# Kernel tuning notes

Measured on AMD Instinct MI355X. Metric: run time of the kernel, lower is better.

The kernel has to match this reference:

```python
import jax, jax.numpy as jnp
import numpy as np
from jax import lax

D_MODEL = 768
D_STATE = 64
BATCH = 2
SEQ = 2048


def setup_inputs() -> dict:
    key = jax.random.key(0)
    ks = jax.random.split(key, 12)
    d, n = D_MODEL, D_STATE
    x = jax.random.normal(ks[0], (BATCH, SEQ, d), dtype=jnp.float32)
    ln_gamma = jnp.ones((d,), jnp.float32)
    ln_beta = jnp.zeros((d,), jnp.float32)
    # nn.Linear default init ~ U(-1/sqrt(d), 1/sqrt(d))
    s = 1.0 / np.sqrt(d)
    W_in = jax.random.uniform(ks[1], (d, d), jnp.float32, -s, s)
    b_in = jax.random.uniform(ks[2], (d,), jnp.float32, -s, s)
    log_A = jax.random.normal(ks[3], (d, n), jnp.float32)
    B_p = jax.random.normal(ks[4], (d, n), jnp.float32) * 0.1
    C_p = jax.random.normal(ks[5], (d, n), jnp.float32) * 0.1
    D_p = jnp.ones((d,), jnp.float32)
    log_dt = jax.random.uniform(ks[6], (d,), jnp.float32) * 0.01 - 2.0
    W_out = jax.random.uniform(ks[7], (d, d), jnp.float32, -s, s)
    b_out = jax.random.uniform(ks[8], (d,), jnp.float32, -s, s)
    return {
        "x": x, "ln_gamma": ln_gamma, "ln_beta": ln_beta,
        "W_in": W_in, "b_in": b_in, "log_A": log_A,
        "B_p": B_p, "C_p": C_p, "D_p": D_p, "log_dt": log_dt,
        "W_out": W_out, "b_out": b_out,
    }


def reference(x, ln_gamma, ln_beta, W_in, b_in, log_A, B_p, C_p, D_p, log_dt, W_out, b_out):
    residual = x
    # LayerNorm (eps=1e-5, elementwise affine)
    mu = jnp.mean(x, axis=-1, keepdims=True)
    var = jnp.var(x, axis=-1, keepdims=True)
    xn = (x - mu) / jnp.sqrt(var + 1e-5) * ln_gamma + ln_beta
    # in_proj (torch Linear: x @ W^T + b)
    u = xn @ W_in.T + b_in  # [B,S,d]
    # Discretization
    A = -jnp.exp(log_A)                     # [d,N]
    dt = jnp.exp(log_dt)[:, None]           # [d,1]
    A_bar = jnp.exp(dt * A)                 # [d,N]
    B_bar = B_p * dt                        # [d,N]
    b, s, d = u.shape
    h0 = jnp.zeros((b, d, D_STATE), u.dtype)
    u_t = jnp.transpose(u, (1, 0, 2))       # [S,B,d]

    def step(h, xt):
        # h: [B,d,N], xt: [B,d]
        h = A_bar * h + B_bar * xt[:, :, None]
        y = jnp.einsum('bdn,dn->bd', h, C_p) + D_p * xt
        return h, y

    _, ys = lax.scan(step, h0, u_t)         # ys: [S,B,d]
    y = jnp.transpose(ys, (1, 0, 2))        # [B,S,d]
    y = y @ W_out.T + b_out
    # dropout is identity in eval mode
    return y + residual
```

## Files before the change

kernel.cpp:

```cpp
#include <hip/hip_runtime.h>
#include <math.h>

#define D_MODEL 768
#define D_STATE 64
#define BATCH   2
#define SEQ     2048
#define M_TOTAL (BATCH * SEQ)

typedef unsigned short ushort_t;
typedef float f32x4 __attribute__((ext_vector_type(4)));
typedef __bf16 bf16x8 __attribute__((ext_vector_type(8)));

__device__ __forceinline__ ushort_t f2bf(float f) {
    unsigned u = __float_as_uint(f);
    u = (u + 0x7FFFu + ((u >> 16) & 1u)) >> 16;
    return (ushort_t)u;
}

__device__ __forceinline__ void gload16(const void* g, void* shm) {
    __builtin_amdgcn_global_load_lds(
        (const __attribute__((address_space(1))) void*)g,
        (__attribute__((address_space(3))) void*)shm, 16, 0, 0);
}

__global__ __launch_bounds__(256) void pre_kernel(const float* __restrict__ x,
                                                  const float* __restrict__ gamma,
                                                  const float* __restrict__ beta,
                                                  ushort_t* __restrict__ xnb,
                                                  const float* __restrict__ W_in,
                                                  const float* __restrict__ W_out,
                                                  ushort_t* __restrict__ Winb,
                                                  ushort_t* __restrict__ Woutb) {
    int bx = blockIdx.x;
    if (bx >= 1024) {
        int b2 = bx - 1024;
        const float* src = (b2 < 576) ? W_in : W_out;
        ushort_t*    dst = (b2 < 576) ? Winb : Woutb;
        int blk = (b2 < 576) ? b2 : b2 - 576;
        int i = (blk * 256 + threadIdx.x) * 4;
        float4 v = *(const float4*)(src + i);
        ushort4 o = make_ushort4(f2bf(v.x), f2bf(v.y), f2bf(v.z), f2bf(v.w));
        *(ushort4*)(dst + i) = o;
        return;
    }
    int row  = bx * 4 + (threadIdx.x >> 6);
    int lane = threadIdx.x & 63;
    const float* xr = x + (size_t)row * D_MODEL;
    float4 v[3];
    v[0] = *(const float4*)(xr + lane * 4);
    v[1] = *(const float4*)(xr + 256 + lane * 4);
    v[2] = *(const float4*)(xr + 512 + lane * 4);
    float s = 0.f, ss = 0.f;
#pragma unroll
    for (int i = 0; i < 3; ++i) {
        s  += v[i].x + v[i].y + v[i].z + v[i].w;
        ss += v[i].x * v[i].x + v[i].y * v[i].y + v[i].z * v[i].z + v[i].w * v[i].w;
    }
#pragma unroll
    for (int off = 1; off < 64; off <<= 1) {
        s  += __shfl_xor(s, off, 64);
        ss += __shfl_xor(ss, off, 64);
    }
    float mean = s * (1.0f / 768.0f);
    float var  = ss * (1.0f / 768.0f) - mean * mean;
    float inv  = 1.0f / sqrtf(var + 1e-5f);
    ushort_t* xo = xnb + (size_t)row * D_MODEL;
#pragma unroll
    for (int i = 0; i < 3; ++i) {
        int c = i * 256 + lane * 4;
        float4 g  = *(const float4*)(gamma + c);
        float4 bb = *(const float4*)(beta + c);
        ushort4 o = make_ushort4(f2bf((v[i].x - mean) * inv * g.x + bb.x),
                                 f2bf((v[i].y - mean) * inv * g.y + bb.y),
                                 f2bf((v[i].z - mean) * inv * g.z + bb.z),
                                 f2bf((v[i].w - mean) * inv * g.w + bb.w));
        *(ushort4*)(xo + c) = o;
    }
}


__global__ __launch_bounds__(256) void gemm_in(const ushort_t* __restrict__ A,
                                               const ushort_t* __restrict__ B,
                                               const float* __restrict__ bias,
                                               ushort_t* __restrict__ uTb) {
    __shared__ __align__(16) char smem[32768];
    float* T = (float*)smem;

    int tid = threadIdx.x;
    int w = tid >> 6, l = tid & 63;
    int bm = blockIdx.x * 64, bn = blockIdx.y * 64;
    int mq = (w & 1) * 32, nq = (w >> 1) * 32;

    int rowq = l >> 4;
    int segq = l & 15;

    float biasv[2];
#pragma unroll
    for (int nt = 0; nt < 2; ++nt)
        biasv[nt] = bias[bn + nq + nt * 16 + (l & 15)];

    f32x4 acc[2][2] = {};
    for (int k0 = 0; k0 < D_MODEL; k0 += 128) {
#pragma unroll
        for (int q = 0; q < 4; ++q) {
            int row = w * 16 + q * 4 + rowq;
            int col = k0 + ((segq ^ (row & 7)) * 8);
            gload16(A + (size_t)(bm + row) * D_MODEL + col, smem + w * 4096 + q * 1024);
            gload16(B + (size_t)(bn + row) * D_MODEL + col, smem + 16384 + w * 4096 + q * 1024);
        }
        __syncthreads();
#pragma unroll
        for (int kk = 0; kk < 4; ++kk) {
            int sgb = kk * 4 + (l >> 4);
            bf16x8 af[2], bf[2];
#pragma unroll
            for (int mt = 0; mt < 2; ++mt) {
                int r = mq + mt * 16 + (l & 15);
                af[mt] = *(const bf16x8*)(smem + r * 256 + ((sgb ^ (r & 7)) * 16));
            }
#pragma unroll
            for (int nt = 0; nt < 2; ++nt) {
                int r = nq + nt * 16 + (l & 15);
                bf[nt] = *(const bf16x8*)(smem + 16384 + r * 256 + ((sgb ^ (r & 7)) * 16));
            }
#pragma unroll
            for (int mt = 0; mt < 2; ++mt)
#pragma unroll
                for (int nt = 0; nt < 2; ++nt)
                    acc[mt][nt] = __builtin_amdgcn_mfma_f32_16x16x32_bf16(af[mt], bf[nt], acc[mt][nt], 0, 0, 0);
        }
        __syncthreads();
    }
#pragma unroll
    for (int mt = 0; mt < 2; ++mt)
#pragma unroll
        for (int nt = 0; nt < 2; ++nt)
#pragma unroll
            for (int i = 0; i < 4; ++i) {
                int nl = nq + nt * 16 + (l & 15);
                int ml = mq + mt * 16 + (l >> 4) * 4 + i;
                T[nl * 68 + ml] = acc[mt][nt][i] + biasv[nt];
            }
    __syncthreads();
    int b = bm >> 11, sbase = bm & 2047;
    int n = tid >> 2, mseg = (tid & 3) * 16;
    ushort_t* dst = uTb + ((size_t)b * D_MODEL + bn + n) * SEQ + sbase + mseg;
#pragma unroll
    for (int q = 0; q < 4; ++q) {
        float4 v = *(const float4*)&T[n * 68 + mseg + q * 4];
        ushort4 o = make_ushort4(f2bf(v.x), f2bf(v.y), f2bf(v.z), f2bf(v.w));
        *(ushort4*)(dst + q * 4) = o;
    }
}

__global__ __launch_bounds__(256) void gemm_out(const ushort_t* __restrict__ A,
                                                const ushort_t* __restrict__ B,
                                                const float* __restrict__ bias,
                                                const float* __restrict__ resid,
                                                float* __restrict__ out) {
    __shared__ __align__(16) char smem[32768];
    int tid = threadIdx.x;
    int w = tid >> 6, l = tid & 63;
    int bm = blockIdx.x * 64, bn = blockIdx.y * 64;
    int mq = (w & 1) * 32, nq = (w >> 1) * 32;

    int rowq = l >> 4;
    int segq = l & 15;

    float biasv[2];
#pragma unroll
    for (int nt = 0; nt < 2; ++nt)
        biasv[nt] = bias[bn + nq + nt * 16 + (l & 15)];

    f32x4 acc[2][2] = {};
    for (int k0 = 0; k0 < D_MODEL; k0 += 128) {
#pragma unroll
        for (int q = 0; q < 4; ++q) {
            int row = w * 16 + q * 4 + rowq;
            int col = k0 + ((segq ^ (row & 7)) * 8);
            gload16(A + (size_t)(bm + row) * D_MODEL + col, smem + w * 4096 + q * 1024);
            gload16(B + (size_t)(bn + row) * D_MODEL + col, smem + 16384 + w * 4096 + q * 1024);
        }
        __syncthreads();
#pragma unroll
        for (int kk = 0; kk < 4; ++kk) {
            int sgb = kk * 4 + (l >> 4);
            bf16x8 af[2], bf[2];
#pragma unroll
            for (int mt = 0; mt < 2; ++mt) {
                int r = mq + mt * 16 + (l & 15);
                af[mt] = *(const bf16x8*)(smem + r * 256 + ((sgb ^ (r & 7)) * 16));
            }
#pragma unroll
            for (int nt = 0; nt < 2; ++nt) {
                int r = nq + nt * 16 + (l & 15);
                bf[nt] = *(const bf16x8*)(smem + 16384 + r * 256 + ((sgb ^ (r & 7)) * 16));
            }
#pragma unroll
            for (int mt = 0; mt < 2; ++mt)
#pragma unroll
                for (int nt = 0; nt < 2; ++nt)
                    acc[mt][nt] = __builtin_amdgcn_mfma_f32_16x16x32_bf16(af[mt], bf[nt], acc[mt][nt], 0, 0, 0);
        }
        __syncthreads();
    }
#pragma unroll
    for (int mt = 0; mt < 2; ++mt)
#pragma unroll
        for (int i = 0; i < 4; ++i) {
            int m = bm + mq + mt * 16 + (l >> 4) * 4 + i;
            const float* rp = resid + (size_t)m * D_MODEL + bn;
            float* op = out + (size_t)m * D_MODEL + bn;
#pragma unroll
            for (int nt = 0; nt < 2; ++nt) {
                int nl = nq + nt * 16 + (l & 15);
                op[nl] = acc[mt][nt][i] + biasv[nt] + rp[nl];
            }
        }
}

#define OFF_U  0
#define OFF_V  9216
#define OFF_T  18432
#define OFF_M  27648
#define OFF_H  36864
#define OFF_W  46080
#define OFF_SM 63488

__global__ __launch_bounds__(256) void scan_mm(const ushort_t* __restrict__ uTb,
                                               const float* __restrict__ log_A,
                                               const float* __restrict__ B_p,
                                               const float* __restrict__ C_p,
                                               const float* __restrict__ D_p,
                                               const float* __restrict__ log_dt,
                                               float* __restrict__ yT) {
    __shared__ __align__(16) char smem[65024];
    ushort_t* Up = (ushort_t*)(smem + OFF_U);
    ushort_t* Vp = (ushort_t*)(smem + OFF_V);
    ushort_t* Tp = (ushort_t*)(smem + OFF_T);
    ushort_t* Mp = (ushort_t*)(smem + OFF_M);
    ushort_t* Hp = (ushort_t*)(smem + OFF_H);
    float*    Wp = (float*)(smem + OFF_W);
    float*    Kp = (float*)(smem + OFF_W);
    float*    aArr  = (float*)(smem + OFF_SM);
    float*    BbArr = aArr + 64;
    float*    CcArr = aArr + 128;
    float*    CBArr = aArr + 192;
    float*    Kc    = aArr + 256;

    int d   = blockIdx.x;
    int tid = threadIdx.x;
    int w   = tid >> 6, l = tid & 63;

    if (tid < 64) {
        int n = tid;
        float dt = __expf(log_dt[d]);
        float a  = -dt * __expf(log_A[d * 64 + n]);
        float Bb = B_p[d * 64 + n] * dt;
        float Cc = C_p[d * 64 + n];
        aArr[n] = a; BbArr[n] = Bb; CcArr[n] = Cc; CBArr[n] = Cc * Bb;
    }
    __syncthreads();

    {
        int tau = tid & 63, part = tid >> 6;
        float s = 0.f;
#pragma unroll
        for (int i = 0; i < 16; ++i) {
            int n = part * 16 + i;
            s += CBArr[n] * __expf((float)tau * aArr[n]);
        }
        Kp[part * 64 + tau] = s;
    }
    __syncthreads();
    if (tid < 64)
        Kc[tid] = Kp[tid] + Kp[64 + tid] + Kp[128 + tid] + Kp[192 + tid]
                + (tid == 0 ? D_p[d] : 0.f);
    __syncthreads();

    {
        int r = tid >> 2, seg = (tid & 3) * 16;
        float a = aArr[r], Bb = BbArr[r];
#pragma unroll
        for (int i = 0; i < 16; ++i) {
            int s = seg + i;
            Vp[r * 72 + s] = f2bf(Bb * __expf((float)(63 - s) * a));
        }
#pragma unroll
        for (int i = 0; i < 16; ++i) {
            int n = seg + i;
            Mp[r * 72 + n] = f2bf(CcArr[n] * __expf((float)(r + 1) * aArr[n]));
        }
#pragma unroll
        for (int i = 0; i < 16; ++i) {
            int s = seg + i;
            Tp[r * 72 + s] = (s <= r) ? f2bf(Kc[r - s]) : (ushort_t)0;
        }
        int col = r, bu = col >> 5, cu = col & 31;
        const ushort_t* usrc = uTb + ((size_t)bu * D_MODEL + d) * SEQ + cu * 64 + seg;
        *(uint4*)(Up + col * 72 + seg)     = *(const uint4*)(usrc);
        *(uint4*)(Up + col * 72 + seg + 8) = *(const uint4*)(usrc + 8);
    }
    __syncthreads();

    {
        int p0 = w * 16;
        f32x4 acc1[4] = {};
#pragma unroll
        for (int kk = 0; kk < 2; ++kk) {
            int koff = kk * 32 + (l >> 4) * 8;
            bf16x8 af = *(const bf16x8*)(Vp + (p0 + (l & 15)) * 72 + koff);
#pragma unroll
            for (int qt = 0; qt < 4; ++qt) {
                bf16x8 bf = *(const bf16x8*)(Up + (qt * 16 + (l & 15)) * 72 + koff);
                acc1[qt] = __builtin_amdgcn_mfma_f32_16x16x32_bf16(af, bf, acc1[qt], 0, 0, 0);
            }
        }
#pragma unroll
        for (int qt = 0; qt < 4; ++qt)
#pragma unroll
            for (int i = 0; i < 4; ++i)
                Wp[(qt * 16 + (l & 15)) * 68 + p0 + (l >> 4) * 4 + i] = acc1[qt][i];
    }
    __syncthreads();

    if (tid < 128) {
        int b2 = tid >> 6, n = tid & 63;
        float Ab64 = __expf(64.f * aArr[n]);
        float H = 0.f;
#pragma unroll
        for (int c = 0; c < 32; ++c) {
            int col = b2 * 32 + c;
            Hp[col * 72 + n] = f2bf(H);
            H = fmaf(Ab64, H, Wp[col * 68 + n]);
        }
    }
    __syncthreads();

    {
        int j0 = w * 16;
        f32x4 accY[4] = {};
#pragma unroll
        for (int kk = 0; kk < 2; ++kk) {
            int koff = kk * 32 + (l >> 4) * 8;
            bf16x8 at = *(const bf16x8*)(Tp + (j0 + (l & 15)) * 72 + koff);
            bf16x8 am = *(const bf16x8*)(Mp + (j0 + (l & 15)) * 72 + koff);
#pragma unroll
            for (int qt = 0; qt < 4; ++qt) {
                bf16x8 bu = *(const bf16x8*)(Up + (qt * 16 + (l & 15)) * 72 + koff);
                bf16x8 bh = *(const bf16x8*)(Hp + (qt * 16 + (l & 15)) * 72 + koff);
                accY[qt] = __builtin_amdgcn_mfma_f32_16x16x32_bf16(at, bu, accY[qt], 0, 0, 0);
                accY[qt] = __builtin_amdgcn_mfma_f32_16x16x32_bf16(am, bh, accY[qt], 0, 0, 0);
            }
        }
#pragma unroll
        for (int qt = 0; qt < 4; ++qt)
#pragma unroll
            for (int i = 0; i < 4; ++i)
                Wp[(qt * 16 + (l & 15)) * 68 + j0 + (l >> 4) * 4 + i] = accY[qt][i];
    }
    __syncthreads();

    {
        int col = tid >> 2, jseg = (tid & 3) * 16;
        int b3 = col >> 5, c3 = col & 31;
        float* dst = yT + ((size_t)b3 * D_MODEL + d) * SEQ + c3 * 64 + jseg;
#pragma unroll
        for (int q = 0; q < 4; ++q)
            *(float4*)(dst + q * 4) = *(const float4*)(Wp + col * 68 + jseg + q * 4);
    }
}

__global__ __launch_bounds__(256) void tcast_kernel(const float* __restrict__ yT,
                                                    ushort_t* __restrict__ yA) {
    __shared__ float T2[64 * 68];
    int t = threadIdx.x;
    int s0 = blockIdx.x * 64, d0 = blockIdx.y * 64, b = blockIdx.z;
    int dl = t >> 2, sq = (t & 3) * 16;
    const float* src = yT + ((size_t)b * D_MODEL + d0 + dl) * SEQ + s0 + sq;
#pragma unroll
    for (int q = 0; q < 4; ++q) {
        float4 v = *(const float4*)(src + q * 4);
        T2[(sq + q * 4 + 0) * 68 + dl] = v.x;
        T2[(sq + q * 4 + 1) * 68 + dl] = v.y;
        T2[(sq + q * 4 + 2) * 68 + dl] = v.z;
        T2[(sq + q * 4 + 3) * 68 + dl] = v.w;
    }
    __syncthreads();
    int sl = t >> 2, dseg = (t & 3) * 16;
    ushort_t* dst = yA + ((size_t)(b * SEQ + s0 + sl)) * D_MODEL + d0 + dseg;
#pragma unroll
    for (int q = 0; q < 4; ++q) {
        float4 v = *(const float4*)&T2[sl * 68 + dseg + q * 4];
        ushort4 o = make_ushort4(f2bf(v.x), f2bf(v.y), f2bf(v.z), f2bf(v.w));
        *(ushort4*)(dst + q * 4) = o;
    }
}

extern "C" void kernel_launch(void* const* d_in, const int* in_sizes, int n_in,
                              void* d_out, int out_size, void* d_ws, size_t ws_size,
                              hipStream_t stream) {
    const float* x        = (const float*)d_in[0];
    const float* ln_gamma = (const float*)d_in[1];
    const float* ln_beta  = (const float*)d_in[2];
    const float* W_in     = (const float*)d_in[3];
    const float* b_in     = (const float*)d_in[4];
    const float* log_A    = (const float*)d_in[5];
    const float* B_p      = (const float*)d_in[6];
    const float* C_p      = (const float*)d_in[7];
    const float* D_p      = (const float*)d_in[8];
    const float* log_dt   = (const float*)d_in[9];
    const float* W_out    = (const float*)d_in[10];
    const float* b_out    = (const float*)d_in[11];
    float* out = (float*)d_out;

    char* ws = (char*)d_ws;
    ushort_t* uTb   = (ushort_t*)(ws + 0);
    float*    yT    = (float*)(ws + 6291456);
    ushort_t* xnb   = (ushort_t*)(ws + 18874368);
    ushort_t* yA    = xnb;
    ushort_t* Winb  = (ushort_t*)(ws + 25165824);
    ushort_t* Woutb = (ushort_t*)(ws + 26345472);

    pre_kernel<<<dim3(1024 + 1152), 256, 0, stream>>>(x, ln_gamma, ln_beta, xnb,
                                                      W_in, W_out, Winb, Woutb);
    gemm_in<<<dim3(M_TOTAL / 64, D_MODEL / 64), 256, 0, stream>>>(xnb, Winb, b_in, uTb);
    scan_mm<<<dim3(D_MODEL), 256, 0, stream>>>(uTb, log_A, B_p, C_p, D_p, log_dt, yT);
    tcast_kernel<<<dim3(SEQ / 64, D_MODEL / 64, BATCH), 256, 0, stream>>>(yT, yA);
    gemm_out<<<dim3(M_TOTAL / 64, D_MODEL / 64), 256, 0, stream>>>(yA, Woutb, b_out, x, out);
}
```

Baseline: 129.2 us.

## Use double-buffered 128x96 GEMM tiles and store scan output as bf16

Both projection GEMMs now share a core that uses larger 128x96 block tiles with 64x48 per-wave tiles and double-buffers the K=64 slices in LDS, so the next slice is prefetched while the current one is multiplied. This raises per-block data reuse and hides global load latency, at the cost of more registers, fewer blocks (256 vs 768) and a launch bound of one block per CU. The scan kernel now writes its transposed output as bf16 instead of fp32, halving that intermediate's traffic and simplifying the transpose kernel to a pure bf16 shuffle. The gemm_in epilogue also converts to bf16 in LDS before wider 16-byte stores.

```diff
diff --git a/kernel.cpp b/kernel.cpp
--- a/kernel.cpp
+++ b/kernel.cpp
@@ -78,143 +78,124 @@
     }
 }
 
-
-__global__ __launch_bounds__(256) void gemm_in(const ushort_t* __restrict__ A,
-                                               const ushort_t* __restrict__ B,
-                                               const float* __restrict__ bias,
-                                               ushort_t* __restrict__ uTb) {
-    __shared__ __align__(16) char smem[32768];
-    float* T = (float*)smem;
-
+#define ABUF  16384
+#define BUFSZ 28672
+
+__device__ __forceinline__ void gemm_core(const ushort_t* __restrict__ A,
+                                          const ushort_t* __restrict__ B,
+                                          const float* __restrict__ bias,
+                                          char* smem, int tid, int bm, int bn,
+                                          int w, int l, int wm, int wn,
+                                          f32x4 acc[4][3], float biasv[3]) {
+    int seg8 = ((l & 7) ^ (l >> 3)) * 8;
+    const ushort_t* gA = A + (size_t)(bm + w * 32 + (l >> 3)) * D_MODEL + seg8;
+    const ushort_t* gB = B + (size_t)(bn + w * 24 + (l >> 3)) * D_MODEL + seg8;
+#pragma unroll
+    for (int nt = 0; nt < 3; ++nt)
+        biasv[nt] = bias[bn + wn + nt * 16 + (l & 15)];
+#pragma unroll
+    for (int q = 0; q < 4; ++q)
+        gload16(gA + (size_t)(q * 8) * D_MODEL, smem + (w * 32 + q * 8) * 128);
+#pragma unroll
+    for (int q = 0; q < 3; ++q)
+        gload16(gB + (size_t)(q * 8) * D_MODEL, smem + ABUF + (w * 24 + q * 8) * 128);
+    __syncthreads();
+    for (int it = 0; it < 12; ++it) {
+        const char* cb = smem + (it & 1) * BUFSZ;
+        if (it < 11) {
+            char* nb = smem + ((it + 1) & 1) * BUFSZ;
+            int k = (it + 1) * 64;
+#pragma unroll
+            for (int q = 0; q < 4; ++q)
+                gload16(gA + (size_t)(q * 8) * D_MODEL + k, nb + (w * 32 + q * 8) * 128);
+#pragma unroll
+            for (int q = 0; q < 3; ++q)
+                gload16(gB + (size_t)(q * 8) * D_MODEL + k, nb + ABUF + (w * 24 + q * 8) * 128);
+        }
+#pragma unroll
+        for (int kk = 0; kk < 2; ++kk) {
+            int sgb = kk * 4 + (l >> 4);
+            bf16x8 af[4], bf[3];
+#pragma unroll
+            for (int mt = 0; mt < 4; ++mt) {
+                int r = wm + mt * 16 + (l & 15);
+                af[mt] = *(const bf16x8*)(cb + r * 128 + ((sgb ^ (r & 7)) * 16));
+            }
+#pragma unroll
+            for (int nt = 0; nt < 3; ++nt) {
+                int r = wn + nt * 16 + (l & 15);
+                bf[nt] = *(const bf16x8*)(cb + ABUF + r * 128 + ((sgb ^ (r & 7)) * 16));
+            }
+#pragma unroll
+            for (int mt = 0; mt < 4; ++mt)
+#pragma unroll
+                for (int nt = 0; nt < 3; ++nt)
+                    acc[mt][nt] = __builtin_amdgcn_mfma_f32_16x16x32_bf16(af[mt], bf[nt], acc[mt][nt], 0, 0, 0);
+        }
+        __syncthreads();
+    }
+}
+
+__global__ __launch_bounds__(256, 1) void gemm_in(const ushort_t* __restrict__ A,
+                                                  const ushort_t* __restrict__ B,
+                                                  const float* __restrict__ bias,
+                                                  ushort_t* __restrict__ uTb) {
+    __shared__ __align__(16) char smem[2 * BUFSZ];
     int tid = threadIdx.x;
     int w = tid >> 6, l = tid & 63;
-    int bm = blockIdx.x * 64, bn = blockIdx.y * 64;
-    int mq = (w & 1) * 32, nq = (w >> 1) * 32;
-
-    int rowq = l >> 4;
-    int segq = l & 15;
-
-    float biasv[2];
-#pragma unroll
-    for (int nt = 0; nt < 2; ++nt)
-        biasv[nt] = bias[bn + nq + nt * 16 + (l & 15)];
-
-    f32x4 acc[2][2] = {};
-    for (int k0 = 0; k0 < D_MODEL; k0 += 128) {
-#pragma unroll
-        for (int q = 0; q < 4; ++q) {
-            int row = w * 16 + q * 4 + rowq;
-            int col = k0 + ((segq ^ (row & 7)) * 8);
-            gload16(A + (size_t)(bm + row) * D_MODEL + col, smem + w * 4096 + q * 1024);
-            gload16(B + (size_t)(bn + row) * D_MODEL + col, smem + 16384 + w * 4096 + q * 1024);
-        }
-        __syncthreads();
-#pragma unroll
-        for (int kk = 0; kk < 4; ++kk) {
-            int sgb = kk * 4 + (l >> 4);
-            bf16x8 af[2], bf[2];
-#pragma unroll
-            for (int mt = 0; mt < 2; ++mt) {
-                int r = mq + mt * 16 + (l & 15);
-                af[mt] = *(const bf16x8*)(smem + r * 256 + ((sgb ^ (r & 7)) * 16));
-            }
-#pragma unroll
-            for (int nt = 0; nt < 2; ++nt) {
-                int r = nq + nt * 16 + (l & 15);
-                bf[nt] = *(const bf16x8*)(smem + 16384 + r * 256 + ((sgb ^ (r & 7)) * 16));
-            }
-#pragma unroll
-            for (int mt = 0; mt < 2; ++mt)
-#pragma unroll
-                for (int nt = 0; nt < 2; ++nt)
-                    acc[mt][nt] = __builtin_amdgcn_mfma_f32_16x16x32_bf16(af[mt], bf[nt], acc[mt][nt], 0, 0, 0);
-        }
-        __syncthreads();
-    }
-#pragma unroll
-    for (int mt = 0; mt < 2; ++mt)
-#pragma unroll
-        for (int nt = 0; nt < 2; ++nt)
+    int bm = blockIdx.x * 128, bn = blockIdx.y * 96;
+    int wm = (w & 1) * 64, wn = (w >> 1) * 48;
+    f32x4 acc[4][3] = {};
+    float biasv[3];
+    gemm_core(A, B, bias, smem, tid, bm, bn, w, l, wm, wn, acc, biasv);
+
+    ushort_t* T = (ushort_t*)smem;
+#pragma unroll
+    for (int mt = 0; mt < 4; ++mt)
+#pragma unroll
+        for (int nt = 0; nt < 3; ++nt)
 #pragma unroll
             for (int i = 0; i < 4; ++i) {
-                int nl = nq + nt * 16 + (l & 15);
-                int ml = mq + mt * 16 + (l >> 4) * 4 + i;
-                T[nl * 68 + ml] = acc[mt][nt][i] + biasv[nt];
-            }
-    __syncthreads();
-    int b = bm >> 11, sbase = bm & 2047;
-    int n = tid >> 2, mseg = (tid & 3) * 16;
-    ushort_t* dst = uTb + ((size_t)b * D_MODEL + bn + n) * SEQ + sbase + mseg;
-#pragma unroll
-    for (int q = 0; q < 4; ++q) {
-        float4 v = *(const float4*)&T[n * 68 + mseg + q * 4];
-        ushort4 o = make_ushort4(f2bf(v.x), f2bf(v.y), f2bf(v.z), f2bf(v.w));
-        *(ushort4*)(dst + q * 4) = o;
-    }
-}
-
-__global__ __launch_bounds__(256) void gemm_out(const ushort_t* __restrict__ A,
-                                                const ushort_t* __restrict__ B,
-                                                const float* __restrict__ bias,
-                                                const float* __restrict__ resid,
-                                                float* __restrict__ out) {
-    __shared__ __align__(16) char smem[32768];
+                int n = wn + nt * 16 + (l & 15);
+                int m = wm + mt * 16 + (l >> 4) * 4 + i;
+                T[n * 136 + m] = f2bf(acc[mt][nt][i] + biasv[nt]);
+            }
+    __syncthreads();
+    int b = bm >> 11, s0 = bm & 2047;
+#pragma unroll
+    for (int rep = 0; rep < 6; ++rep) {
+        int idx = rep * 256 + tid;
+        int row = idx >> 4, sg = idx & 15;
+        uint4 v = *(const uint4*)&T[row * 136 + sg * 8];
+        *(uint4*)(uTb + ((size_t)b * D_MODEL + bn + row) * SEQ + s0 + sg * 8) = v;
+    }
+}
+
+__global__ __launch_bounds__(256, 1) void gemm_out(const ushort_t* __restrict__ A,
+                                                   const ushort_t* __restrict__ B,
+                                                   const float* __restrict__ bias,
+                                                   const float* __restrict__ resid,
+                                                   float* __restrict__ out) {
+    __shared__ __align__(16) char smem[2 * BUFSZ];
     int tid = threadIdx.x;
     int w = tid >> 6, l = tid & 63;
-    int bm = blockIdx.x * 64, bn = blockIdx.y * 64;
-    int mq = (w & 1) * 32, nq = (w >> 1) * 32;
-
-    int rowq = l >> 4;
-    int segq = l & 15;
-
-    float biasv[2];
-#pragma unroll
-    for (int nt = 0; nt < 2; ++nt)
-        biasv[nt] = bias[bn + nq + nt * 16 + (l & 15)];
-
-    f32x4 acc[2][2] = {};
-    for (int k0 = 0; k0 < D_MODEL; k0 += 128) {
-#pragma unroll
-        for (int q = 0; q < 4; ++q) {
-            int row = w * 16 + q * 4 + rowq;
-            int col = k0 + ((segq ^ (row & 7)) * 8);
-            gload16(A + (size_t)(bm + row) * D_MODEL + col, smem + w * 4096 + q * 1024);
-            gload16(B + (size_t)(bn + row) * D_MODEL + col, smem + 16384 + w * 4096 + q * 1024);
-        }
-        __syncthreads();
-#pragma unroll
-        for (int kk = 0; kk < 4; ++kk) {
-            int sgb = kk * 4 + (l >> 4);
-            bf16x8 af[2], bf[2];
-#pragma unroll
-            for (int mt = 0; mt < 2; ++mt) {
-                int r = mq + mt * 16 + (l & 15);
-                af[mt] = *(const bf16x8*)(smem + r * 256 + ((sgb ^ (r & 7)) * 16));
-            }
-#pragma unroll
-            for (int nt = 0; nt < 2; ++nt) {
-                int r = nq + nt * 16 + (l & 15);
-                bf[nt] = *(const bf16x8*)(smem + 16384 + r * 256 + ((sgb ^ (r & 7)) * 16));
-            }
-#pragma unroll
-            for (int mt = 0; mt < 2; ++mt)
-#pragma unroll
-                for (int nt = 0; nt < 2; ++nt)
-                    acc[mt][nt] = __builtin_amdgcn_mfma_f32_16x16x32_bf16(af[mt], bf[nt], acc[mt][nt], 0, 0, 0);
-        }
-        __syncthreads();
-    }
-#pragma unroll
-    for (int mt = 0; mt < 2; ++mt)
+    int bm = blockIdx.x * 128, bn = blockIdx.y * 96;
+    int wm = (w & 1) * 64, wn = (w >> 1) * 48;
+    f32x4 acc[4][3] = {};
+    float biasv[3];
+    gemm_core(A, B, bias, smem, tid, bm, bn, w, l, wm, wn, acc, biasv);
+
+#pragma unroll
+    for (int mt = 0; mt < 4; ++mt)
 #pragma unroll
         for (int i = 0; i < 4; ++i) {
-            int m = bm + mq + mt * 16 + (l >> 4) * 4 + i;
+            int m = bm + wm + mt * 16 + (l >> 4) * 4 + i;
             const float* rp = resid + (size_t)m * D_MODEL + bn;
             float* op = out + (size_t)m * D_MODEL + bn;
 #pragma unroll
-            for (int nt = 0; nt < 2; ++nt) {
-                int nl = nq + nt * 16 + (l & 15);
-                op[nl] = acc[mt][nt][i] + biasv[nt] + rp[nl];
+            for (int nt = 0; nt < 3; ++nt) {
+                int n = wn + nt * 16 + (l & 15);
+                op[n] = acc[mt][nt][i] + biasv[nt] + rp[n];
             }
         }
 }
@@ -233,7 +214,7 @@
                                                const float* __restrict__ C_p,
                                                const float* __restrict__ D_p,
                                                const float* __restrict__ log_dt,
-                                               float* __restrict__ yT) {
+                                               ushort_t* __restrict__ yTb) {
     __shared__ __align__(16) char smem[65024];
     ushort_t* Up = (ushort_t*)(smem + OFF_U);
     ushort_t* Vp = (ushort_t*)(smem + OFF_V);
@@ -364,37 +345,34 @@
     {
         int col = tid >> 2, jseg = (tid & 3) * 16;
         int b3 = col >> 5, c3 = col & 31;
-        float* dst = yT + ((size_t)b3 * D_MODEL + d) * SEQ + c3 * 64 + jseg;
-#pragma unroll
-        for (int q = 0; q < 4; ++q)
-            *(float4*)(dst + q * 4) = *(const float4*)(Wp + col * 68 + jseg + q * 4);
-    }
-}
-
-__global__ __launch_bounds__(256) void tcast_kernel(const float* __restrict__ yT,
+        ushort_t* dst = yTb + ((size_t)b3 * D_MODEL + d) * SEQ + c3 * 64 + jseg;
+#pragma unroll
+        for (int q = 0; q < 4; ++q) {
+            float4 v = *(const float4*)(Wp + col * 68 + jseg + q * 4);
+            ushort4 o = make_ushort4(f2bf(v.x), f2bf(v.y), f2bf(v.z), f2bf(v.w));
+            *(ushort4*)(dst + q * 4) = o;
+        }
+    }
+}
+
+__global__ __launch_bounds__(256) void tcast_kernel(const ushort_t* __restrict__ yTb,
                                                     ushort_t* __restrict__ yA) {
-    __shared__ float T2[64 * 68];
+    __shared__ ushort_t T3[64 * 72];
     int t = threadIdx.x;
     int s0 = blockIdx.x * 64, d0 = blockIdx.y * 64, b = blockIdx.z;
     int dl = t >> 2, sq = (t & 3) * 16;
-    const float* src = yT + ((size_t)b * D_MODEL + d0 + dl) * SEQ + s0 + sq;
-#pragma unroll
-    for (int q = 0; q < 4; ++q) {
-        float4 v = *(const float4*)(src + q * 4);
-        T2[(sq + q * 4 + 0) * 68 + dl] = v.x;
-        T2[(sq + q * 4 + 1) * 68 + dl] = v.y;
-        T2[(sq + q * 4 + 2) * 68 + dl] = v.z;
-        T2[(sq + q * 4 + 3) * 68 + dl] = v.w;
-    }
+    const ushort_t* src = yTb + ((size_t)b * D_MODEL + d0 + dl) * SEQ + s0 + sq;
+    ushort_t tmp[16];
+    *(uint4*)tmp       = *(const uint4*)src;
+    *(uint4*)(tmp + 8) = *(const uint4*)(src + 8);
+#pragma unroll
+    for (int i = 0; i < 16; ++i)
+        T3[(sq + i) * 72 + dl] = tmp[i];
     __syncthreads();
     int sl = t >> 2, dseg = (t & 3) * 16;
-    ushort_t* dst = yA + ((size_t)(b * SEQ + s0 + sl)) * D_MODEL + d0 + dseg;
-#pragma unroll
-    for (int q = 0; q < 4; ++q) {
-        float4 v = *(const float4*)&T2[sl * 68 + dseg + q * 4];
-        ushort4 o = make_ushort4(f2bf(v.x), f2bf(v.y), f2bf(v.z), f2bf(v.w));
-        *(ushort4*)(dst + q * 4) = o;
-    }
+    ushort_t* dst = yA + ((size_t)b * SEQ + s0 + sl) * D_MODEL + d0 + dseg;
+    *(uint4*)dst       = *(const uint4*)&T3[sl * 72 + dseg];
+    *(uint4*)(dst + 8) = *(const uint4*)&T3[sl * 72 + dseg + 8];
 }
 
 extern "C" void kernel_launch(void* const* d_in, const int* in_sizes, int n_in,
@@ -416,16 +394,16 @@
 
     char* ws = (char*)d_ws;
     ushort_t* uTb   = (ushort_t*)(ws + 0);
-    float*    yT    = (float*)(ws + 6291456);
-    ushort_t* xnb   = (ushort_t*)(ws + 18874368);
+    ushort_t* yTb   = (ushort_t*)(ws + 6291456);
+    ushort_t* xnb   = (ushort_t*)(ws + 12582912);
     ushort_t* yA    = xnb;
-    ushort_t* Winb  = (ushort_t*)(ws + 25165824);
-    ushort_t* Woutb = (ushort_t*)(ws + 26345472);
+    ushort_t* Winb  = (ushort_t*)(ws + 18874368);
+    ushort_t* Woutb = (ushort_t*)(ws + 20054016);
 
     pre_kernel<<<dim3(1024 + 1152), 256, 0, stream>>>(x, ln_gamma, ln_beta, xnb,
                                                       W_in, W_out, Winb, Woutb);
-    gemm_in<<<dim3(M_TOTAL / 64, D_MODEL / 64), 256, 0, stream>>>(xnb, Winb, b_in, uTb);
-    scan_mm<<<dim3(D_MODEL), 256, 0, stream>>>(uTb, log_A, B_p, C_p, D_p, log_dt, yT);
-    tcast_kernel<<<dim3(SEQ / 64, D_MODEL / 64, BATCH), 256, 0, stream>>>(yT, yA);
-    gemm_out<<<dim3(M_TOTAL / 64, D_MODEL / 64), 256, 0, stream>>>(yA, Woutb, b_out, x, out);
-}
+    gemm_in<<<dim3(M_TOTAL / 128, D_MODEL / 96), 256, 0, stream>>>(xnb, Winb, b_in, uTb);
+    scan_mm<<<dim3(D_MODEL), 256, 0, stream>>>(uTb, log_A, B_p, C_p, D_p, log_dt, yTb);
+    tcast_kernel<<<dim3(SEQ / 64, D_MODEL / 64, BATCH), 256, 0, stream>>>(yTb, yA);
+    gemm_out<<<dim3(M_TOTAL / 128, D_MODEL / 96), 256, 0, stream>>>(yA, Woutb, b_out, x, out);
+}
```

After: 129.8 us. Within noise of the previous version (+0.5%).
